# Kernel optimization log

Hardware: AMD Instinct MI355X
Metric: run time of the kernel (lower is better)

The kernel has to match this reference:

```python
import jax, jax.numpy as jnp
import numpy as np

H, W = 512, 512
STRIDE = 4
SCALE_RATIO = 32.0
POST_MIN = 2.0
POST_MAX = 100.0
BG_RATIO = 0.15
CUT_OFF = 100.0


def setup_inputs() -> dict:
    key = jax.random.key(0)
    k1, k2, k3, k4 = jax.random.split(key, 4)
    B, N = 8, 256
    scale = jax.random.uniform(k1, (B, N, 2), dtype=jnp.float32)          # raw scales in [0,1)
    rotation = jax.random.normal(k2, (B, N, 1), dtype=jnp.float32)        # rotation angle per point
    points = jax.random.uniform(k3, (B, N, 2), dtype=jnp.float32,
                                minval=0.0, maxval=float(W))              # head coords in image
    st_sizes = jax.random.uniform(k4, (B,), dtype=jnp.float32,
                                  minval=256.0, maxval=512.0)             # unused in math (as in torch)
    return {"scale": scale, "rotation": rotation, "points": points, "st_sizes": st_sizes}


def reference(scale, rotation, points, st_sizes):
    # grid centers, meshgrid indexing='xy' -> (H/stride, W/stride)
    xx = jnp.arange(0, W, STRIDE, dtype=jnp.float32) + STRIDE / 2
    yy = jnp.arange(0, H, STRIDE, dtype=jnp.float32) + STRIDE / 2
    gx, gy = jnp.meshgrid(xx, yy, indexing='xy')
    gx = gx.reshape(-1)   # (HW,)
    gy = gy.reshape(-1)

    # per-point anisotropic scales, clamped as in torch
    s = jnp.clip(SCALE_RATIO * scale, STRIDE / POST_MIN, POST_MAX)        # (B,N,2)
    sx2 = s[..., 0] ** 2                                                  # (B,N)
    sy2 = s[..., 1] ** 2

    th = rotation[..., 0]
    c, si = jnp.cos(th), jnp.sin(th)
    # covariance = R diag(sx2, sy2) R^T  (2x2 symmetric, closed form)
    cov_a = c * c * sx2 + si * si * sy2
    cov_b = c * si * (sx2 - sy2)
    cov_d = si * si * sx2 + c * c * sy2
    det = sx2 * sy2                                                       # det(cov), (B,N)
    inv_a = cov_d / det
    inv_b = -cov_b / det
    inv_d = cov_a / det

    # displacement from each grid center to each point: (B,N,HW)
    dx = gx[None, None, :] - points[..., 0:1]
    dy = gy[None, None, :] - points[..., 1:2]

    # z = -0.5 * xy^T inv_cov xy
    z = -0.5 * (inv_a[..., None] * dx * dx
                + 2.0 * inv_b[..., None] * dx * dy
                + inv_d[..., None] * dy * dy)                             # (B,N,HW)

    likelihood = z - 0.5 * jnp.log(det)[..., None]

    # background likelihood (use_bg and cut_off set)
    min_z = jnp.max(z, axis=1)                                            # (B,HW)
    idx = jnp.argmax(z, axis=1)                                           # (B,HW)
    d_const = -0.5 * CUT_OFF * CUT_OFF
    bk_z = d_const - min_z
    det_sel = jnp.take_along_axis(det, idx, axis=1)                       # (B,HW)
    bk_like = bk_z - jnp.log(det_sel / BG_RATIO)

    likelihood = jnp.concatenate([likelihood, bk_like[:, None, :]], axis=1)  # (B,N+1,HW)
    return jax.nn.softmax(likelihood, axis=1)
```

## Files before the change

### kernel.cpp

```cpp
#include <hip/hip_runtime.h>


#define HWC 16384
#define NPTS 256
#define NBATCH 8

#define K_LOG2E 1.4426950408889634f
#define BK_CONST (-7216.2121700389835f)

__global__ __launch_bounds__(256) void prep_kernel(
    const float* __restrict__ scale,
    const float* __restrict__ rotation,
    const float* __restrict__ points,
    float4* __restrict__ P)
{
    const int i = blockIdx.x * 256 + threadIdx.x;
    if (i >= NBATCH * NPTS) return;

    float sx = fminf(fmaxf(32.0f * scale[i * 2 + 0], 2.0f), 100.0f);
    float sy = fminf(fmaxf(32.0f * scale[i * 2 + 1], 2.0f), 100.0f);
    float sx2 = sx * sx, sy2 = sy * sy;

    float th = rotation[i];
    float s, c;
    sincosf(th, &s, &c);
    float cov_a = c * c * sx2 + s * s * sy2;
    float cov_b = c * s * (sx2 - sy2);
    float cov_d = s * s * sx2 + c * c * sy2;
    float det  = sx2 * sy2;
    float rdet = 1.0f / det;

    float KA = -0.5f * K_LOG2E * (cov_d * rdet);
    float KB =         K_LOG2E * (cov_b * rdet);
    float KD = -0.5f * K_LOG2E * (cov_a * rdet);

    float px = points[i * 2 + 0];
    float py = points[i * 2 + 1];

    float cx = -(2.0f * KA * px + KB * py);
    float cy = -(KB * px + 2.0f * KD * py);
    float cz = KA * px * px + KB * px * py + KD * py * py;

    float l2det = log2f(det);
    float HLK = -0.5f * l2det;

    P[i * 2 + 0] = make_float4(KA, KB, KD, cx);
    P[i * 2 + 1] = make_float4(cy, cz + HLK, HLK, l2det);
}

#define LIKE(q0, q1) fmaf((q0).x, gxx, fmaf((q0).y, gxy, fmaf((q0).z, gyy, \
                     fmaf((q0).w, gx,  fmaf((q1).x, gy, (q1).y)))))

__global__ __launch_bounds__(512) void post_prob_kernel(
    const float4* __restrict__ P,
    float* __restrict__ out)
{
    __shared__ float sM[512];
    __shared__ float sBZ[512];
    __shared__ float sBLD[512];
    __shared__ float sS[512];

    const int b      = blockIdx.x >> 8;
    const int hwbase = (blockIdx.x & 255) << 6;
    const int tid    = threadIdx.x;
    const int h      = tid & 63;
    const int hw     = hwbase + h;
    const int g      = __builtin_amdgcn_readfirstlane(tid >> 6);

    const float gx = (float)((hw & 127) * 4 + 2);
    const float gy = (float)((hw >> 7) * 4 + 2);
    const float gxx = gx * gx, gxy = gx * gy, gyy = gy * gy;

    const float4* __restrict__ Pb = P + (b * NPTS + g * 32) * 2;

    float lk[32];
    float m = -INFINITY, bz = -INFINITY, bld = 0.0f;
    #pragma unroll
    for (int i = 0; i < 32; ++i) {
        float4 q0 = Pb[i * 2 + 0];
        float4 q1 = Pb[i * 2 + 1];
        float like = LIKE(q0, q1);
        lk[i] = like;
        m = fmaxf(m, like);
        float z = like - q1.z;
        bool gt = z > bz;
        bz  = gt ? z    : bz;
        bld = gt ? q1.w : bld;
    }
    sM[tid] = m; sBZ[tid] = bz; sBLD[tid] = bld;
    __syncthreads();

    float mf = sM[h], bzf = sBZ[h], bldf = sBLD[h];
    #pragma unroll
    for (int q = 1; q < 8; ++q) {
        mf = fmaxf(mf, sM[h + q * 64]);
        float zq = sBZ[h + q * 64];
        bool gt = zq > bzf;
        bzf  = gt ? zq : bzf;
        bldf = gt ? sBLD[h + q * 64] : bldf;
    }
    const float bk = BK_CONST - bzf - bldf;
    mf = fmaxf(mf, bk);

    float s = 0.0f;
    #pragma unroll
    for (int i = 0; i < 32; ++i) {
        float e = exp2f(lk[i] - mf);
        lk[i] = e;
        s += e;
    }
    sS[tid] = s;
    __syncthreads();

    float sum = exp2f(bk - mf);
    #pragma unroll
    for (int q = 0; q < 8; ++q) sum += sS[h + q * 64];
    const float inv = 1.0f / sum;

    float* __restrict__ outb = out + ((size_t)b * 257 + g * 32) * HWC + hw;
    #pragma unroll
    for (int i = 0; i < 32; ++i)
        outb[(size_t)i * HWC] = lk[i] * inv;

    if (tid < 64)
        out[((size_t)b * 257 + 256) * HWC + hw] = exp2f(bk - mf) * inv;
}

extern "C" void kernel_launch(void* const* d_in, const int* in_sizes, int n_in,
                              void* d_out, int out_size, void* d_ws, size_t ws_size,
                              hipStream_t stream) {
    const float* scale    = (const float*)d_in[0];
    const float* rotation = (const float*)d_in[1];
    const float* points   = (const float*)d_in[2];
    float* out = (float*)d_out;
    float4* P  = (float4*)d_ws;
    (void)in_sizes; (void)n_in; (void)out_size; (void)ws_size;

    prep_kernel<<<dim3(NBATCH), dim3(256), 0, stream>>>(scale, rotation, points, P);
    post_prob_kernel<<<dim3(NBATCH * (HWC / 64)), dim3(512), 0, stream>>>(P, out);
}
```

Measured before the change: 146.3 us.

## Split softmax into reduce pass and separate vectorized recompute-and-store kernel

The fused kernel becomes two. A reduction kernel computes each pixel's log-sum-exp (max plus log2 of the sum) and writes it to workspace along with the background channel. A separate store kernel then recomputes each point's likelihood per row-contiguous chunk and writes exp2(like - lse) with float4 stores. This aims to get coalesced, vectorized output writes and to stop holding 32 likelihoods in registers, at the cost of recomputing the quadratic form, an extra launch and an extra workspace round trip.

New measurement: 162.4 us. 1.11x slower.

```diff
diff --git a/kernel.cpp b/kernel.cpp
--- a/kernel.cpp
+++ b/kernel.cpp
@@ -51,8 +51,9 @@
 #define LIKE(q0, q1) fmaf((q0).x, gxx, fmaf((q0).y, gxy, fmaf((q0).z, gyy, \
                      fmaf((q0).w, gx,  fmaf((q1).x, gy, (q1).y)))))
 
-__global__ __launch_bounds__(512) void post_prob_kernel(
+__global__ __launch_bounds__(512) void reduce_kernel(
     const float4* __restrict__ P,
+    float* __restrict__ m2arr,
     float* __restrict__ out)
 {
     __shared__ float sM[512];
@@ -73,14 +74,12 @@
 
     const float4* __restrict__ Pb = P + (b * NPTS + g * 32) * 2;
 
-    float lk[32];
     float m = -INFINITY, bz = -INFINITY, bld = 0.0f;
-    #pragma unroll
+    #pragma unroll 8
     for (int i = 0; i < 32; ++i) {
         float4 q0 = Pb[i * 2 + 0];
         float4 q1 = Pb[i * 2 + 1];
         float like = LIKE(q0, q1);
-        lk[i] = like;
         m = fmaxf(m, like);
         float z = like - q1.z;
         bool gt = z > bz;
@@ -103,11 +102,11 @@
     mf = fmaxf(mf, bk);
 
     float s = 0.0f;
-    #pragma unroll
+    #pragma unroll 8
     for (int i = 0; i < 32; ++i) {
-        float e = exp2f(lk[i] - mf);
-        lk[i] = e;
-        s += e;
+        float4 q0 = Pb[i * 2 + 0];
+        float4 q1 = Pb[i * 2 + 1];
+        s += exp2f(LIKE(q0, q1) - mf);
     }
     sS[tid] = s;
     __syncthreads();
@@ -115,15 +114,48 @@
     float sum = exp2f(bk - mf);
     #pragma unroll
     for (int q = 0; q < 8; ++q) sum += sS[h + q * 64];
-    const float inv = 1.0f / sum;
+    const float m2 = mf + log2f(sum);
 
-    float* __restrict__ outb = out + ((size_t)b * 257 + g * 32) * HWC + hw;
+    if (tid < 64) {
+        m2arr[b * HWC + hw] = m2;
+        out[((size_t)b * 257 + 256) * HWC + hw] = exp2f(bk - m2);
+    }
+}
+
+__global__ __launch_bounds__(256) void store_kernel(
+    const float4* __restrict__ P,
+    const float* __restrict__ m2arr,
+    float* __restrict__ out)
+{
+    const int bid   = blockIdx.x;
+    const int bn    = bid >> 4;
+    const int chunk = bid & 15;
+    const int b     = bn >> 8;
+    const int tid   = threadIdx.x;
+    const int hw    = chunk * 1024 + tid * 4;
+
+    float4 q0 = P[bn * 2 + 0];
+    float4 q1 = P[bn * 2 + 1];
+
+    const int x0 = hw & 127;
+    const float gy = (float)((hw >> 7) * 4 + 2);
+    const float cyt = fmaf(q1.x, gy, q1.y);
+    const float kdy = q0.z * gy * gy;
+    const float base = cyt + kdy;
+
+    float4 mm = *reinterpret_cast<const float4*>(m2arr + b * HWC + hw);
+
+    float e[4];
     #pragma unroll
-    for (int i = 0; i < 32; ++i)
-        outb[(size_t)i * HWC] = lk[i] * inv;
+    for (int j = 0; j < 4; ++j) {
+        float gx = (float)((x0 + j) * 4 + 2);
+        float like = fmaf(fmaf(q0.x, gx, fmaf(q0.y, gy, q0.w)), gx, base);
+        float mj = (j == 0) ? mm.x : (j == 1) ? mm.y : (j == 2) ? mm.z : mm.w;
+        e[j] = exp2f(like - mj);
+    }
 
-    if (tid < 64)
-        out[((size_t)b * 257 + 256) * HWC + hw] = exp2f(bk - mf) * inv;
+    float* dst = out + (size_t)(bn + b) * HWC + hw;
+    *reinterpret_cast<float4*>(dst) = make_float4(e[0], e[1], e[2], e[3]);
 }
 
 extern "C" void kernel_launch(void* const* d_in, const int* in_sizes, int n_in,
@@ -134,8 +166,10 @@
     const float* points   = (const float*)d_in[2];
     float* out = (float*)d_out;
     float4* P  = (float4*)d_ws;
+    float* m2  = (float*)((char*)d_ws + 65536);
     (void)in_sizes; (void)n_in; (void)out_size; (void)ws_size;
 
     prep_kernel<<<dim3(NBATCH), dim3(256), 0, stream>>>(scale, rotation, points, P);
-    post_prob_kernel<<<dim3(NBATCH * (HWC / 64)), dim3(512), 0, stream>>>(P, out);
+    reduce_kernel<<<dim3(NBATCH * (HWC / 64)), dim3(512), 0, stream>>>(P, m2, out);
+    store_kernel<<<dim3(NBATCH * NPTS * 16), dim3(256), 0, stream>>>(P, m2, out);
 }
```

## Process four pixels per thread with float4 stores and recompute likelihoods

Applied to the files above, without the earlier changes.

Each thread now handles four horizontally adjacent grid cells, and the y-dependent terms of the quadratic are factored out and shared across them. The 32-entry likelihood array is no longer kept in registers; likelihoods are recomputed in each of three passes (max, sum, write), and the division is folded into the exponent through log2 of the sum. Output is written with 128-bit stores. The grid shrinks from 2048 blocks to 512, which lowers occupancy and parallelism in exchange for wider stores and fewer live registers, at the cost of extra ALU work from recomputation.

Result: slower. 173.6 us (+18.7%).

```diff
diff --git a/kernel.cpp b/kernel.cpp
--- a/kernel.cpp
+++ b/kernel.cpp
@@ -48,82 +48,133 @@
     P[i * 2 + 1] = make_float4(cy, cz + HLK, HLK, l2det);
 }
 
-#define LIKE(q0, q1) fmaf((q0).x, gxx, fmaf((q0).y, gxy, fmaf((q0).z, gyy, \
-                     fmaf((q0).w, gx,  fmaf((q1).x, gy, (q1).y)))))
-
-__global__ __launch_bounds__(512) void post_prob_kernel(
+__global__ __launch_bounds__(512) void fused_kernel(
     const float4* __restrict__ P,
     float* __restrict__ out)
 {
-    __shared__ float sM[512];
-    __shared__ float sBZ[512];
-    __shared__ float sBLD[512];
-    __shared__ float sS[512];
+    __shared__ float4 sM[8][64];
+    __shared__ float4 sBZ[8][64];
+    __shared__ float4 sBLD[8][64];
+    __shared__ float4 sS[8][64];
 
-    const int b      = blockIdx.x >> 8;
-    const int hwbase = (blockIdx.x & 255) << 6;
-    const int tid    = threadIdx.x;
-    const int h      = tid & 63;
-    const int hw     = hwbase + h;
-    const int g      = __builtin_amdgcn_readfirstlane(tid >> 6);
+    const int b     = blockIdx.x >> 6;
+    const int chunk = blockIdx.x & 63;
+    const int tid   = threadIdx.x;
+    const int l     = tid & 63;
+    const int g     = __builtin_amdgcn_readfirstlane(tid >> 6);
 
-    const float gx = (float)((hw & 127) * 4 + 2);
-    const float gy = (float)((hw >> 7) * 4 + 2);
-    const float gxx = gx * gx, gxy = gx * gy, gyy = gy * gy;
+    const int hw0 = chunk * 256 + l * 4;
+    const float gy  = (float)((hw0 >> 7) * 4 + 2);
+    const float gx0 = (float)((hw0 & 127) * 4 + 2);
 
-    const float4* __restrict__ Pb = P + (b * NPTS + g * 32) * 2;
+    const float4* __restrict__ Pg = P + (b * NPTS + g * 32) * 2;
 
-    float lk[32];
-    float m = -INFINITY, bz = -INFINITY, bld = 0.0f;
+    float m[4], bz[4], bld[4];
     #pragma unroll
+    for (int j = 0; j < 4; ++j) { m[j] = -INFINITY; bz[j] = -INFINITY; bld[j] = 0.0f; }
+
+    #pragma unroll 4
     for (int i = 0; i < 32; ++i) {
-        float4 q0 = Pb[i * 2 + 0];
-        float4 q1 = Pb[i * 2 + 1];
-        float like = LIKE(q0, q1);
-        lk[i] = like;
-        m = fmaxf(m, like);
-        float z = like - q1.z;
-        bool gt = z > bz;
-        bz  = gt ? z    : bz;
-        bld = gt ? q1.w : bld;
+        float4 q0 = Pg[i * 2 + 0];
+        float4 q1 = Pg[i * 2 + 1];
+        float gcoef = fmaf(q0.y, gy, q0.w);
+        float base  = fmaf(fmaf(q0.z, gy, q1.x), gy, q1.y);
+        #pragma unroll
+        for (int j = 0; j < 4; ++j) {
+            float gx = gx0 + 4.0f * j;
+            float like = fmaf(fmaf(q0.x, gx, gcoef), gx, base);
+            m[j] = fmaxf(m[j], like);
+            float z = like - q1.z;
+            bool gt = z > bz[j];
+            bz[j]  = gt ? z    : bz[j];
+            bld[j] = gt ? q1.w : bld[j];
+        }
     }
-    sM[tid] = m; sBZ[tid] = bz; sBLD[tid] = bld;
+    sM[g][l]   = make_float4(m[0], m[1], m[2], m[3]);
+    sBZ[g][l]  = make_float4(bz[0], bz[1], bz[2], bz[3]);
+    sBLD[g][l] = make_float4(bld[0], bld[1], bld[2], bld[3]);
     __syncthreads();
 
-    float mf = sM[h], bzf = sBZ[h], bldf = sBLD[h];
+    float mf[4], bzf[4], bldf[4];
+    {
+        float4 m0 = sM[0][l], z0 = sBZ[0][l], d0 = sBLD[0][l];
+        mf[0]=m0.x; mf[1]=m0.y; mf[2]=m0.z; mf[3]=m0.w;
+        bzf[0]=z0.x; bzf[1]=z0.y; bzf[2]=z0.z; bzf[3]=z0.w;
+        bldf[0]=d0.x; bldf[1]=d0.y; bldf[2]=d0.z; bldf[3]=d0.w;
+        #pragma unroll
+        for (int q = 1; q < 8; ++q) {
+            float4 mq = sM[q][l], zq = sBZ[q][l], dq = sBLD[q][l];
+            const float mqa[4] = {mq.x, mq.y, mq.z, mq.w};
+            const float zqa[4] = {zq.x, zq.y, zq.z, zq.w};
+            const float dqa[4] = {dq.x, dq.y, dq.z, dq.w};
+            #pragma unroll
+            for (int j = 0; j < 4; ++j) {
+                mf[j] = fmaxf(mf[j], mqa[j]);
+                bool gt = zqa[j] > bzf[j];
+                bzf[j]  = gt ? zqa[j] : bzf[j];
+                bldf[j] = gt ? dqa[j] : bldf[j];
+            }
+        }
+    }
+    float bk[4];
     #pragma unroll
-    for (int q = 1; q < 8; ++q) {
-        mf = fmaxf(mf, sM[h + q * 64]);
-        float zq = sBZ[h + q * 64];
-        bool gt = zq > bzf;
-        bzf  = gt ? zq : bzf;
-        bldf = gt ? sBLD[h + q * 64] : bldf;
+    for (int j = 0; j < 4; ++j) {
+        bk[j] = BK_CONST - bzf[j] - bldf[j];
+        mf[j] = fmaxf(mf[j], bk[j]);
     }
-    const float bk = BK_CONST - bzf - bldf;
-    mf = fmaxf(mf, bk);
 
-    float s = 0.0f;
-    #pragma unroll
+    float s[4] = {0.0f, 0.0f, 0.0f, 0.0f};
+    #pragma unroll 4
     for (int i = 0; i < 32; ++i) {
-        float e = exp2f(lk[i] - mf);
-        lk[i] = e;
-        s += e;
+        float4 q0 = Pg[i * 2 + 0];
+        float4 q1 = Pg[i * 2 + 1];
+        float gcoef = fmaf(q0.y, gy, q0.w);
+        float base  = fmaf(fmaf(q0.z, gy, q1.x), gy, q1.y);
+        #pragma unroll
+        for (int j = 0; j < 4; ++j) {
+            float gx = gx0 + 4.0f * j;
+            float like = fmaf(fmaf(q0.x, gx, gcoef), gx, base);
+            s[j] += exp2f(like - mf[j]);
+        }
     }
-    sS[tid] = s;
+    sS[g][l] = make_float4(s[0], s[1], s[2], s[3]);
     __syncthreads();
 
-    float sum = exp2f(bk - mf);
+    float sum[4];
     #pragma unroll
-    for (int q = 0; q < 8; ++q) sum += sS[h + q * 64];
-    const float inv = 1.0f / sum;
+    for (int j = 0; j < 4; ++j) sum[j] = exp2f(bk[j] - mf[j]);
+    #pragma unroll
+    for (int q = 0; q < 8; ++q) {
+        float4 sq = sS[q][l];
+        sum[0] += sq.x; sum[1] += sq.y; sum[2] += sq.z; sum[3] += sq.w;
+    }
+    float m2[4];
+    #pragma unroll
+    for (int j = 0; j < 4; ++j) m2[j] = mf[j] + log2f(sum[j]);
 
-    float* __restrict__ outb = out + ((size_t)b * 257 + g * 32) * HWC + hw;
-    #pragma unroll
-    for (int i = 0; i < 32; ++i)
-        outb[(size_t)i * HWC] = lk[i] * inv;
-
-    if (tid < 64)
-        out[((size_t)b * 257 + 256) * HWC + hw] = exp2f(bk - mf) * inv;
+    float* __restrict__ dst = out + ((size_t)b * 257 + g * 32) * HWC + hw0;
+    #pragma unroll 4
+    for (int i = 0; i < 32; ++i) {
+        float4 q0 = Pg[i * 2 + 0];
+        float4 q1 = Pg[i * 2 + 1];
+        float gcoef = fmaf(q0.y, gy, q0.w);
+        float base  = fmaf(fmaf(q0.z, gy, q1.x), gy, q1.y);
+        float4 e;
+        float gx;
+        gx = gx0;         e.x = exp2f(fmaf(fmaf(q0.x, gx, gcoef), gx, base) - m2[0]);
+        gx = gx0 + 4.0f;  e.y = exp2f(fmaf(fmaf(q0.x, gx, gcoef), gx, base) - m2[1]);
+        gx = gx0 + 8.0f;  e.z = exp2f(fmaf(fmaf(q0.x, gx, gcoef), gx, base) - m2[2]);
+        gx = gx0 + 12.0f; e.w = exp2f(fmaf(fmaf(q0.x, gx, gcoef), gx, base) - m2[3]);
+        *reinterpret_cast<float4*>(dst + (size_t)i * HWC) = e;
+    }
+    if (g == 0) {
+        float4 e;
+        e.x = exp2f(bk[0] - m2[0]);
+        e.y = exp2f(bk[1] - m2[1]);
+        e.z = exp2f(bk[2] - m2[2]);
+        e.w = exp2f(bk[3] - m2[3]);
+        *reinterpret_cast<float4*>(out + ((size_t)b * 257 + 256) * HWC + hw0) = e;
+    }
 }
 
 extern "C" void kernel_launch(void* const* d_in, const int* in_sizes, int n_in,
@@ -137,5 +188,5 @@
     (void)in_sizes; (void)n_in; (void)out_size; (void)ws_size;
 
     prep_kernel<<<dim3(NBATCH), dim3(256), 0, stream>>>(scale, rotation, points, P);
-    post_prob_kernel<<<dim3(NBATCH * (HWC / 64)), dim3(512), 0, stream>>>(P, out);
+    fused_kernel<<<dim3(NBATCH * 64), dim3(512), 0, stream>>>(P, out);
 }
```
